# Kernel optimization log

Hardware: AMD Instinct MI355X
Metric: run time of the kernel (lower is better)

Reference implementation:

```python
import jax, jax.numpy as jnp
import numpy as np

N_USER, N_ITEM = 60000, 60000
N = N_USER + N_ITEM
E_BASE = 1500000
P = 200000
IN_DIM, HID, OUT = 128, 128, 64
K_MAX = 0.5


def setup_inputs() -> dict:
    key = jax.random.key(0)
    ks = jax.random.split(key, 20)
    feat_user = jax.random.normal(ks[0], (N_USER, 256), jnp.float32)
    feat_item = jax.random.normal(ks[1], (N_ITEM, 128), jnp.float32)
    src_b = jax.random.randint(ks[2], (E_BASE,), 0, N, jnp.int32)
    dst_b = jax.random.randint(ks[3], (E_BASE,), 0, N, jnp.int32)
    loops = jnp.arange(N, dtype=jnp.int32)  # dgl.add_self_loop
    src = jnp.concatenate([src_b, loops])
    dst = jnp.concatenate([dst_b, loops])
    pos_src = jax.random.randint(ks[4], (P,), 0, N, jnp.int32)
    pos_dst = jax.random.randint(ks[5], (P,), 0, N, jnp.int32)
    neg_src = jax.random.randint(ks[6], (P,), 0, N, jnp.int32)
    neg_dst = jax.random.randint(ks[7], (P,), 0, N, jnp.int32)
    s = 0.05
    W_user = jax.random.normal(ks[8], (256, IN_DIM), jnp.float32) * s
    b_user = jnp.zeros((IN_DIM,), jnp.float32)
    W_item = jax.random.normal(ks[9], (128, IN_DIM), jnp.float32) * s
    b_item = jnp.zeros((IN_DIM,), jnp.float32)
    W_gat = jax.random.normal(ks[10], (IN_DIM, HID), jnp.float32) * s
    attn_l = jax.random.normal(ks[11], (HID,), jnp.float32) * s
    attn_r = jax.random.normal(ks[12], (HID,), jnp.float32) * s
    gat_bias = jnp.zeros((HID,), jnp.float32)
    W_pred = jax.random.normal(ks[13], (HID, OUT), jnp.float32) * s
    b_pred = jnp.zeros((OUT,), jnp.float32)
    return {
        "feat_user": feat_user, "feat_item": feat_item,
        "W_user": W_user, "b_user": b_user, "W_item": W_item, "b_item": b_item,
        "W_gat": W_gat, "attn_l": attn_l, "attn_r": attn_r, "gat_bias": gat_bias,
        "W_pred": W_pred, "b_pred": b_pred,
        "src": src, "dst": dst,
        "pos_src": pos_src, "pos_dst": pos_dst,
        "neg_src": neg_src, "neg_dst": neg_dst,
        "alpha_T": 1,
    }


def _gat_conv(x, src, dst, W_gat, attn_l, attn_r, gat_bias):
    # DGL GATConv, 1 head: fc (no bias), additive attention, edge softmax over dst.
    z = x @ W_gat                              # [N, HID]
    el = z @ attn_l                            # [N]
    er = z @ attn_r                            # [N]
    e = jax.nn.leaky_relu(el[src] + er[dst], 0.2)   # [E]
    m = jax.ops.segment_max(e, dst, num_segments=N)  # per-dst max (self loops -> no empty segs)
    ex = jnp.exp(e - m[dst])
    ssum = jax.ops.segment_sum(ex, dst, num_segments=N)
    a = ex / ssum[dst]                          # edge softmax coeffs
    msg = z[src] * a[:, None]                   # [E, HID]
    out = jax.ops.segment_sum(msg, dst, num_segments=N) + gat_bias
    return jax.nn.elu(out)                      # activation=F.elu


def _hold_loss(score, k_T):
    l = jax.nn.log_sigmoid(score)
    hold = k_T * jnp.max(l)
    l = jnp.where(l > hold, 0.0, l)
    return -jnp.sum(l)


def reference(feat_user, feat_item, W_user, b_user, W_item, b_item,
              W_gat, attn_l, attn_r, gat_bias, W_pred, b_pred,
              src, dst, pos_src, pos_dst, neg_src, neg_dst, alpha_T):
    # per-type input projection then concat in ntype order (dgl.to_homogeneous)
    hu = feat_user @ W_user + b_user
    hi = feat_item @ W_item + b_item
    x = jnp.concatenate([hu, hi], axis=0)       # [N, IN_DIM]
    h = _gat_conv(x, src, dst, W_gat, attn_l, attn_r, gat_bias)
    pos_score = jnp.sum(h[pos_src] * h[pos_dst], axis=1)
    neg_score = jnp.sum(h[neg_src] * h[neg_dst], axis=1)
    k_T = K_MAX if K_MAX <= alpha_T else alpha_T   # k_T = min(k_max, alpha_T)
    loss = _hold_loss(pos_score, k_T) + _hold_loss(neg_score, k_T)
    out = h[:N_USER] @ W_pred + b_pred          # predict_type 'user' == type id 0
    return loss, out
```

## Files before the change

kernel.cpp:

```cpp
#include <hip/hip_runtime.h>
#include <hip/hip_bf16.h>
#include <math.h>

#define NUSER 60000
#define NITEM 60000
#define NNODE 120000
#define BSH 9
#define NB 235
#define CAP 8192

typedef __attribute__((ext_vector_type(8))) short bf16x8;
typedef __attribute__((ext_vector_type(4))) float f32x4;
typedef __attribute__((ext_vector_type(2))) float f32x2;
typedef __attribute__((ext_vector_type(4))) unsigned short u16x4;

__device__ __forceinline__ float leaky02(float x) { return x > 0.f ? x : 0.2f * x; }

__device__ __forceinline__ float inv_ord(unsigned int u) {
  unsigned int bits = (u & 0x80000000u) ? (u & 0x7FFFFFFFu) : ~u;
  return __uint_as_float(bits);
}
__device__ __forceinline__ unsigned int ord_of(float f) {
  unsigned int u = __float_as_uint(f);
  return (u & 0x80000000u) ? ~u : (u | 0x80000000u);
}
__device__ __forceinline__ short f2bs(float f) {
  __hip_bfloat16 h = __float2bfloat16(f);
  return *reinterpret_cast<short*>(&h);
}

__device__ __forceinline__ void f8fma(f32x2& acc, float w, unsigned int u) {
  f32x2 zz = __builtin_amdgcn_cvt_pk_f32_fp8(u, false);
  f32x2 ww; ww.x = w; ww.y = w;
  acc = __builtin_elementwise_fma(ww, zz, acc);
}
__device__ __forceinline__ void fp8dot(f32x2& acc, unsigned int ua, unsigned int ub) {
  f32x2 a0 = __builtin_amdgcn_cvt_pk_f32_fp8(ua, false);
  f32x2 a1 = __builtin_amdgcn_cvt_pk_f32_fp8(ua, true);
  f32x2 b0 = __builtin_amdgcn_cvt_pk_f32_fp8(ub, false);
  f32x2 b1 = __builtin_amdgcn_cvt_pk_f32_fp8(ub, true);
  acc = __builtin_elementwise_fma(a0, b0, acc);
  acc = __builtin_elementwise_fma(a1, b1, acc);
}

__global__ __launch_bounds__(256) void prep_count_kernel(
    const float* __restrict__ Wu, const float* __restrict__ bu, const float* __restrict__ Wi,
    const float* __restrict__ bi, const float* __restrict__ Wg, const float* __restrict__ Wp,
    __hip_bfloat16* __restrict__ Bp_u, __hip_bfloat16* __restrict__ Bp_i,
    __hip_bfloat16* __restrict__ Bp_p, float* __restrict__ bf_u, float* __restrict__ bf_i,
    const int* __restrict__ dst, int* __restrict__ btotal, int E) {
  __shared__ int cnt[NB];
  if (blockIdx.x < 512) {
    int bid = blockIdx.x;
    for (int t = threadIdx.x; t < NB; t += 256) cnt[t] = 0;
    __syncthreads();
    for (int i = bid * 256 + threadIdx.x; i < E; i += 512 * 256)
      atomicAdd(&cnt[dst[i] >> BSH], 1);
    __syncthreads();
    for (int t = threadIdx.x; t < NB; t += 256)
      if (cnt[t]) atomicAdd(&btotal[t], cnt[t]);
    return;
  }
  int t = (blockIdx.x - 512) * 256 + threadIdx.x;
  if (t < 32768) {
    int j = t & 7, lane = (t >> 3) & 63, rest = t >> 9;
    int nt = rest & 7, ks = rest >> 3;
    int k = ks * 32 + ((lane >> 4) << 3) + j;
    int n = nt * 16 + (lane & 15);
    float acc = 0.f;
#pragma unroll 8
    for (int jj = 0; jj < 128; ++jj) acc = fmaf(Wu[k * 128 + jj], Wg[jj * 128 + n], acc);
    Bp_u[t] = __float2bfloat16(acc);
  } else if (t < 49152) {
    int tt = t - 32768;
    int j = tt & 7, lane = (tt >> 3) & 63, rest = tt >> 9;
    int nt = rest & 7, ks = rest >> 3;
    int k = ks * 32 + ((lane >> 4) << 3) + j;
    int n = nt * 16 + (lane & 15);
    float acc = 0.f;
#pragma unroll 8
    for (int jj = 0; jj < 128; ++jj) acc = fmaf(Wi[k * 128 + jj], Wg[jj * 128 + n], acc);
    Bp_i[tt] = __float2bfloat16(acc);
  } else if (t < 57344) {
    int tt = t - 49152;
    int j = tt & 7, lane = (tt >> 3) & 63, rest = tt >> 9;
    int nt = rest & 3, ks = rest >> 2;
    int k = ks * 32 + ((lane >> 4) << 3) + j;
    int n = nt * 16 + (lane & 15);
    Bp_p[tt] = __float2bfloat16(Wp[k * 64 + n]);
  } else if (t < 57344 + 256) {
    int n = t - 57344;
    if (n < 128) {
      float acc = 0.f;
      for (int jj = 0; jj < 128; ++jj) acc = fmaf(bu[jj], Wg[jj * 128 + n], acc);
      bf_u[n] = acc;
    } else {
      int nn = n - 128;
      float acc = 0.f;
      for (int jj = 0; jj < 128; ++jj) acc = fmaf(bi[jj], Wg[jj * 128 + nn], acc);
      bf_i[nn] = acc;
    }
  }
}

__global__ void bscan_kernel(const int* __restrict__ btotal, int* __restrict__ bstart,
                             int* __restrict__ gcur) {
  __shared__ int s[256];
  int t = threadIdx.x;
  int v = (t < NB) ? btotal[t] : 0;
  s[t] = v;
  __syncthreads();
  for (int off = 1; off < 256; off <<= 1) {
    int a = (t >= off) ? s[t - off] : 0;
    __syncthreads();
    s[t] += a;
    __syncthreads();
  }
  int excl = s[t] - v;
  if (t < NB) { bstart[t] = excl; gcur[t] = excl; }
  if (t == NB - 1) bstart[NB] = s[t];
}

template <int K>
__device__ __forceinline__ void zgemm_body(
    char* smem, const float* __restrict__ A, const __hip_bfloat16* __restrict__ Bp,
    const float* __restrict__ bias, const float* __restrict__ al, const float* __restrict__ ar,
    unsigned char* __restrict__ z8, float* __restrict__ el, float* __restrict__ er, int M,
    int blk) {
  const int lane = threadIdx.x & 63, wv = threadIdx.x >> 6;
  const int t = threadIdx.x;
  int arow = blk * 64 + wv * 16 + (lane & 15);
  if (arow >= M) arow = M - 1;
  const float* a0 = A + (size_t)arow * K + ((lane >> 4) << 3);
  const bf16x8* bp = (const bf16x8*)Bp;
  f32x4 acc[8] = {};
#pragma unroll
  for (int ks = 0; ks < K / 32; ++ks) {
    float4 a1 = *(const float4*)(a0 + ks * 32);
    float4 a2 = *(const float4*)(a0 + ks * 32 + 4);
    bf16x8 af;
    af[0] = f2bs(a1.x); af[1] = f2bs(a1.y); af[2] = f2bs(a1.z); af[3] = f2bs(a1.w);
    af[4] = f2bs(a2.x); af[5] = f2bs(a2.y); af[6] = f2bs(a2.z); af[7] = f2bs(a2.w);
#pragma unroll
    for (int nt = 0; nt < 8; ++nt) {
      bf16x8 bfr = bp[(ks * 8 + nt) * 64 + lane];
      acc[nt] = __builtin_amdgcn_mfma_f32_16x16x32_bf16(af, bfr, acc[nt], 0, 0, 0);
    }
  }
  float(*lds2)[68] = (float(*)[68])smem;
  int row = t >> 2, qq = t & 3;
  int gm = blk * 64 + row;
  float pl = 0.f, pr = 0.f;
#pragma unroll
  for (int p = 0; p < 2; ++p) {
    __syncthreads();
#pragma unroll
    for (int nt = p * 4; nt < p * 4 + 4; ++nt) {
      float b = bias[nt * 16 + (lane & 15)];
#pragma unroll
      for (int r = 0; r < 4; ++r)
        lds2[wv * 16 + (lane >> 4) * 4 + r][(nt & 3) * 16 + (lane & 15)] = acc[nt][r] + b;
    }
    __syncthreads();
    if (gm < M) {
#pragma unroll
      for (int v4 = 0; v4 < 2; ++v4) {
        float f[8];
#pragma unroll
        for (int j = 0; j < 8; ++j) {
          f[j] = lds2[row][qq * 16 + v4 * 8 + j];
          int c = p * 64 + qq * 16 + v4 * 8 + j;
          pl = fmaf(f[j], al[c], pl);
          pr = fmaf(f[j], ar[c], pr);
        }
        unsigned int w0 = (unsigned int)__builtin_amdgcn_cvt_pk_fp8_f32(f[0], f[1], 0, false);
        w0 = (unsigned int)__builtin_amdgcn_cvt_pk_fp8_f32(f[2], f[3], (int)w0, true);
        unsigned int w1 = (unsigned int)__builtin_amdgcn_cvt_pk_fp8_f32(f[4], f[5], 0, false);
        w1 = (unsigned int)__builtin_amdgcn_cvt_pk_fp8_f32(f[6], f[7], (int)w1, true);
        uint2 st; st.x = w0; st.y = w1;
        *(uint2*)(z8 + (size_t)gm * 128 + p * 64 + qq * 16 + v4 * 8) = st;
      }
    }
  }
  pl += __shfl_xor(pl, 1, 64); pl += __shfl_xor(pl, 2, 64);
  pr += __shfl_xor(pr, 1, 64); pr += __shfl_xor(pr, 2, 64);
  if (qq == 0 && gm < M) { el[gm] = pl; er[gm] = pr; }
}

__global__ __launch_bounds__(256) void zgemm_scatter_kernel(
    const float* __restrict__ Au, const __hip_bfloat16* __restrict__ Bpu,
    const float* __restrict__ bfu, const float* __restrict__ Ai,
    const __hip_bfloat16* __restrict__ Bpi, const float* __restrict__ bfi,
    const float* __restrict__ al, const float* __restrict__ ar, unsigned char* __restrict__ z8,
    float* __restrict__ el, float* __restrict__ er, int SC, int GU,
    const int* __restrict__ src, const int* __restrict__ dst, int* __restrict__ gcur,
    unsigned int* __restrict__ scratch, int E) {
  __shared__ __align__(16) char smem[17408];
  int bx = blockIdx.x;
  if (bx < SC) {
    int* cnt = (int*)smem;
    int* basep = cnt + NB;
    for (int t = threadIdx.x; t < NB; t += 256) cnt[t] = 0;
    __syncthreads();
    const int i0 = bx * 4096;
    unsigned int v_[16];
    int b_[16], r_[16];
#pragma unroll
    for (int j = 0; j < 16; ++j) {
      int i = i0 + j * 256 + threadIdx.x;
      b_[j] = -1;
      if (i < E) {
        int d = dst[i];
        int s = src[i];
        int b = d >> BSH;
        b_[j] = b;
        r_[j] = atomicAdd(&cnt[b], 1);
        v_[j] = (unsigned int)s | ((unsigned int)(d & 511) << 17);
      }
    }
    __syncthreads();
    for (int t = threadIdx.x; t < NB; t += 256)
      basep[t] = cnt[t] ? atomicAdd(&gcur[t], cnt[t]) : 0;
    __syncthreads();
#pragma unroll
    for (int j = 0; j < 16; ++j)
      if (b_[j] >= 0) scratch[basep[b_[j]] + r_[j]] = v_[j];
    return;
  }
  int gb = bx - SC;
  if (gb < GU)
    zgemm_body<256>(smem, Au, Bpu, bfu, al, ar, z8, el, er, NUSER, gb);
  else
    zgemm_body<128>(smem, Ai, Bpi, bfi, al, ar, z8 + (size_t)NUSER * 128, el + NUSER, er + NUSER,
                    NITEM, gb - GU);
}

__global__ __launch_bounds__(512) void bsort_kernel(const unsigned int* __restrict__ scratch,
                                                    const int* __restrict__ bstart,
                                                    int* __restrict__ offs, int* __restrict__ ssrc) {
  __shared__ unsigned int buf[CAP];
  __shared__ int cnt[512], scn[512], cur[512];
  int b = blockIdx.x, t = threadIdx.x;
  int s = bstart[b], e = bstart[b + 1], n = e - s;
  int d0 = b << BSH;
  int ndst = NNODE - d0;
  if (ndst > 512) ndst = 512;
  cnt[t] = 0;
  cur[t] = 0;
  __syncthreads();
  bool fit = (n <= CAP);
  if (fit) {
    for (int i = t; i < n; i += 512) {
      unsigned int v = scratch[s + i];
      buf[i] = v;
      atomicAdd(&cnt[v >> 17], 1);
    }
  } else {
    for (int i = t; i < n; i += 512) atomicAdd(&cnt[scratch[s + i] >> 17], 1);
  }
  __syncthreads();
  scn[t] = cnt[t];
  __syncthreads();
  for (int off = 1; off < 512; off <<= 1) {
    int a = (t >= off) ? scn[t - off] : 0;
    __syncthreads();
    scn[t] += a;
    __syncthreads();
  }
  int start = scn[t] - cnt[t];
  if (t < ndst) offs[d0 + t] = s + start;
  if (b == NB - 1 && t == 0) offs[NNODE] = e;
  __syncthreads();
  cnt[t] = start;
  __syncthreads();
  if (fit) {
    for (int i = t; i < n; i += 512) {
      unsigned int v = buf[i];
      int dl = v >> 17;
      int r = atomicAdd(&cur[dl], 1);
      ssrc[s + cnt[dl] + r] = (int)(v & 0x1FFFFu);
    }
  } else {
    for (int i = t; i < n; i += 512) {
      unsigned int v = scratch[s + i];
      int dl = v >> 17;
      int r = atomicAdd(&cur[dl], 1);
      ssrc[s + cnt[dl] + r] = (int)(v & 0x1FFFFu);
    }
  }
}

__global__ __launch_bounds__(256) void aggregate_kernel(
    const unsigned char* __restrict__ z8, const float* __restrict__ el,
    const float* __restrict__ er, const int* __restrict__ offs, const int* __restrict__ ssrc,
    const float* __restrict__ gat_bias, __hip_bfloat16* __restrict__ h,
    unsigned char* __restrict__ h8) {
  __shared__ __align__(16) float2 ew[4][128];
  int wv = threadIdx.x >> 6, lane = threadIdx.x & 63;
  int d = blockIdx.x * 4 + wv;
  int s0 = offs[d], s1 = offs[d + 1];
  int deg = s1 - s0;
  float erd = er[d];
  const unsigned short* zw = (const unsigned short*)z8;
  f32x2 acc = {0.f, 0.f};
  float ssum = 0.f;
  if (deg <= 128) {
    float w0 = 0.f, w1 = 0.f;
    int o0 = 0, o1 = 0;
    if (lane < deg) { int s = ssrc[s0 + lane]; o0 = s << 6; w0 = __expf(leaky02(el[s] + erd)); }
    if (64 + lane < deg) { int s = ssrc[s0 + 64 + lane]; o1 = s << 6; w1 = __expf(leaky02(el[s] + erd)); }
    ew[wv][lane] = make_float2(w0, __int_as_float(o0));
    ew[wv][64 + lane] = make_float2(w1, __int_as_float(o1));
    __builtin_amdgcn_wave_barrier();
    int i = 0;
    for (; i + 8 <= deg; i += 8) {
      float4 p0 = *(const float4*)&ew[wv][i];
      float4 p1 = *(const float4*)&ew[wv][i + 2];
      float4 p2 = *(const float4*)&ew[wv][i + 4];
      float4 p3 = *(const float4*)&ew[wv][i + 6];
      unsigned int u0 = zw[__float_as_uint(p0.y) + lane];
      unsigned int u1 = zw[__float_as_uint(p0.w) + lane];
      unsigned int u2 = zw[__float_as_uint(p1.y) + lane];
      unsigned int u3 = zw[__float_as_uint(p1.w) + lane];
      unsigned int u4 = zw[__float_as_uint(p2.y) + lane];
      unsigned int u5 = zw[__float_as_uint(p2.w) + lane];
      unsigned int u6 = zw[__float_as_uint(p3.y) + lane];
      unsigned int u7 = zw[__float_as_uint(p3.w) + lane];
      ssum += ((p0.x + p0.z) + (p1.x + p1.z)) + ((p2.x + p2.z) + (p3.x + p3.z));
      f8fma(acc, p0.x, u0); f8fma(acc, p0.z, u1);
      f8fma(acc, p1.x, u2); f8fma(acc, p1.z, u3);
      f8fma(acc, p2.x, u4); f8fma(acc, p2.z, u5);
      f8fma(acc, p3.x, u6); f8fma(acc, p3.z, u7);
    }
    for (; i + 2 <= deg; i += 2) {
      float4 p = *(const float4*)&ew[wv][i];
      unsigned int ua = zw[__float_as_uint(p.y) + lane];
      unsigned int ub = zw[__float_as_uint(p.w) + lane];
      ssum += p.x + p.z;
      f8fma(acc, p.x, ua); f8fma(acc, p.z, ub);
    }
    if (i < deg) {
      float2 pp = ew[wv][i];
      unsigned int u = zw[__float_as_uint(pp.y) + lane];
      ssum += pp.x;
      f8fma(acc, pp.x, u);
    }
  } else {
    for (int i2 = s0; i2 < s1; ++i2) {
      int s = ssrc[i2];
      float w = __expf(leaky02(el[s] + erd));
      ssum += w;
      unsigned int u = zw[((unsigned int)s << 6) + lane];
      f8fma(acc, w, u);
    }
  }
  float inv = 1.f / ssum;
  float o0f = acc.x * inv + gat_bias[lane * 2];
  float o1f = acc.y * inv + gat_bias[lane * 2 + 1];
  o0f = (o0f > 0.f) ? o0f : (__expf(o0f) - 1.f);
  o1f = (o1f > 0.f) ? o1f : (__expf(o1f) - 1.f);
  ushort2 ov;
  ov.x = (unsigned short)((unsigned int)f2bs(o0f) & 0xFFFFu);
  ov.y = (unsigned short)((unsigned int)f2bs(o1f) & 0xFFFFu);
  *(ushort2*)((unsigned short*)h + (size_t)d * 128 + lane * 2) = ov;
  int pk8 = __builtin_amdgcn_cvt_pk_fp8_f32(o0f, o1f, 0, false);
  *(unsigned short*)(h8 + (size_t)d * 128 + lane * 2) = (unsigned short)(pk8 & 0xFFFF);
}

__global__ __launch_bounds__(256) void scorepred_kernel(
    const unsigned char* __restrict__ h8, const int* __restrict__ ps, const int* __restrict__ pd,
    const int* __restrict__ ns, const int* __restrict__ nd, float* __restrict__ l_pos,
    float* __restrict__ l_neg, unsigned int* __restrict__ maxacc, int P,
    const __hip_bfloat16* __restrict__ h, const __hip_bfloat16* __restrict__ Bp,
    const float* __restrict__ bias, float* __restrict__ outp, int GP, int NSB) {
  if ((int)blockIdx.x < GP) {
    const int lane = threadIdx.x & 63, wv = threadIdx.x >> 6;
    const int m0 = blockIdx.x * 64 + wv * 16;
    int arow = m0 + (lane & 15);
    if (arow >= NUSER) arow = NUSER - 1;
    const bf16x8* a0 = (const bf16x8*)(h + (size_t)arow * 128) + (lane >> 4);
    const bf16x8* bp = (const bf16x8*)Bp;
    f32x4 acc[4] = {};
#pragma unroll
    for (int ks = 0; ks < 4; ++ks) {
      bf16x8 af = a0[ks * 4];
#pragma unroll
      for (int nt = 0; nt < 4; ++nt) {
        bf16x8 bfr = bp[(ks * 4 + nt) * 64 + lane];
        acc[nt] = __builtin_amdgcn_mfma_f32_16x16x32_bf16(af, bfr, acc[nt], 0, 0, 0);
      }
    }
#pragma unroll
    for (int nt = 0; nt < 4; ++nt) {
      int col = nt * 16 + (lane & 15);
      float b = bias[col];
#pragma unroll
      for (int r = 0; r < 4; ++r) {
        int m = m0 + (lane >> 4) * 4 + r;
        if (m < NUSER) outp[(size_t)m * 64 + col] = acc[nt][r] + b;
      }
    }
    return;
  }
  const int sb = blockIdx.x - GP;
  const int g8 = threadIdx.x >> 3, l8 = threadIdx.x & 7;
  const uint4* h4 = (const uint4*)h8;
  const int stride = NSB * 32;
  const int tot = 2 * P;
  float mpos = -1e30f, mneg = -1e30f;

  int i = sb * 32 + g8;
  int aC = 0, bC = 0;
  if (i < tot) {
    bool n = i >= P; int j = n ? i - P : i;
    aC = n ? ns[j] : ps[j]; bC = n ? nd[j] : pd[j];
  }
  uint4 vaC = {0, 0, 0, 0}, vbC = {0, 0, 0, 0};
  if (i < tot) {
    vaC = h4[(size_t)aC * 8 + l8];
    vbC = h4[(size_t)bC * 8 + l8];
  }
  int i1 = i + stride;
  int aN = 0, bN = 0;
  if (i1 < tot) {
    bool n = i1 >= P; int j = n ? i1 - P : i1;
    aN = n ? ns[j] : ps[j]; bN = n ? nd[j] : pd[j];
  }

  while (i < tot) {
    uint4 vaN = {0, 0, 0, 0}, vbN = {0, 0, 0, 0};
    if (i1 < tot) {
      vaN = h4[(size_t)aN * 8 + l8];
      vbN = h4[(size_t)bN * 8 + l8];
    }
    int i2 = i1 + stride;
    int aN2 = 0, bN2 = 0;
    if (i2 < tot) {
      bool n = i2 >= P; int j = n ? i2 - P : i2;
      aN2 = n ? ns[j] : ps[j]; bN2 = n ? nd[j] : pd[j];
    }
    f32x2 acc = {0.f, 0.f};
    fp8dot(acc, vaC.x, vbC.x);
    fp8dot(acc, vaC.y, vbC.y);
    fp8dot(acc, vaC.z, vbC.z);
    fp8dot(acc, vaC.w, vbC.w);
    float s = acc.x + acc.y;
    s += __shfl_xor(s, 1, 8);
    s += __shfl_xor(s, 2, 8);
    s += __shfl_xor(s, 4, 8);
    float lv = fminf(s, 0.f) - log1pf(__expf(-fabsf(s)));
    bool neg = i >= P;
    int j = neg ? i - P : i;
    if (l8 == 0) (neg ? l_neg : l_pos)[j] = lv;
    if (neg) mneg = fmaxf(mneg, lv); else mpos = fmaxf(mpos, lv);
    i = i1; i1 = i2;
    aC = aN; bC = bN; aN = aN2; bN = bN2;
    vaC = vaN; vbC = vbN;
  }
  __shared__ float red0[256], red1[256];
  red0[threadIdx.x] = mpos;
  red1[threadIdx.x] = mneg;
  __syncthreads();
  for (int off = 128; off; off >>= 1) {
    if (threadIdx.x < off) {
      red0[threadIdx.x] = fmaxf(red0[threadIdx.x], red0[threadIdx.x + off]);
      red1[threadIdx.x] = fmaxf(red1[threadIdx.x], red1[threadIdx.x + off]);
    }
    __syncthreads();
  }
  if (threadIdx.x == 0) {
    atomicMax(maxacc + 0, ord_of(red0[0]));
    atomicMax(maxacc + 1, ord_of(red1[0]));
  }
}

__global__ __launch_bounds__(256) void loss_sum_kernel(const float* __restrict__ l_pos,
                                                       const float* __restrict__ l_neg,
                                                       const unsigned int* __restrict__ maxacc,
                                                       const int* __restrict__ alpha,
                                                       float* __restrict__ sums,
                                                       unsigned int* __restrict__ fincnt,
                                                       float* __restrict__ out, int P) {
  __shared__ float sdata[256];
  int which = blockIdx.x >> 9;
  const float* l = which ? l_neg : l_pos;
  float a = (float)alpha[0];
  float kT = (0.5f <= a) ? 0.5f : a;
  float hold = kT * inv_ord(maxacc[which]);
  float s = 0.f;
  for (int i = (blockIdx.x & 511) * 256 + threadIdx.x; i < P; i += 512 * 256) {
    float v = l[i];
    if (!(v > hold)) s += v;
  }
  sdata[threadIdx.x] = s;
  __syncthreads();
  for (int off = 128; off; off >>= 1) {
    if (threadIdx.x < off) sdata[threadIdx.x] += sdata[threadIdx.x + off];
    __syncthreads();
  }
  if (threadIdx.x == 0) {
    atomicAdd(&sums[which], sdata[0]);
    __threadfence();
    unsigned int t = atomicAdd(fincnt, 1u);
    if (t == 1023u) {
      float s0 = atomicAdd(&sums[0], 0.f);
      float s1 = atomicAdd(&sums[1], 0.f);
      out[0] = -(s0 + s1);
    }
  }
}

extern "C" void kernel_launch(void* const* d_in, const int* in_sizes, int n_in,
                              void* d_out, int out_size, void* d_ws, size_t ws_size,
                              hipStream_t stream) {
  const float* feat_user = (const float*)d_in[0];
  const float* feat_item = (const float*)d_in[1];
  const float* W_user = (const float*)d_in[2];
  const float* b_user = (const float*)d_in[3];
  const float* W_item = (const float*)d_in[4];
  const float* b_item = (const float*)d_in[5];
  const float* W_gat = (const float*)d_in[6];
  const float* attn_l = (const float*)d_in[7];
  const float* attn_r = (const float*)d_in[8];
  const float* gat_bias = (const float*)d_in[9];
  const float* W_pred = (const float*)d_in[10];
  const float* b_pred = (const float*)d_in[11];
  const int* src = (const int*)d_in[12];
  const int* dst = (const int*)d_in[13];
  const int* pos_src = (const int*)d_in[14];
  const int* pos_dst = (const int*)d_in[15];
  const int* neg_src = (const int*)d_in[16];
  const int* neg_dst = (const int*)d_in[17];
  const int* alpha = (const int*)d_in[18];
  const int E = in_sizes[12];
  const int P = in_sizes[14];

  char* p = (char*)d_ws;
  auto alloc = [&](size_t bytes) {
    char* r = p;
    p += (bytes + 255) & ~(size_t)255;
    return r;
  };
  unsigned char* z8 = (unsigned char*)alloc((size_t)NNODE * 128);
  __hip_bfloat16* h = (__hip_bfloat16*)alloc((size_t)NNODE * 128 * 2);
  unsigned char* h8 = (unsigned char*)alloc((size_t)NNODE * 128);
  float* el = (float*)alloc((size_t)NNODE * 4);
  float* er = (float*)alloc((size_t)NNODE * 4);
  __hip_bfloat16* Bp_u = (__hip_bfloat16*)alloc(256 * 128 * 2);
  __hip_bfloat16* Bp_i = (__hip_bfloat16*)alloc(128 * 128 * 2);
  __hip_bfloat16* Bp_p = (__hip_bfloat16*)alloc(128 * 64 * 2);
  float* bf_u = (float*)alloc(128 * 4);
  float* bf_i = (float*)alloc(128 * 4);
  int* offs = (int*)alloc((size_t)(NNODE + 4) * 4);
  int* ssrc = (int*)alloc((size_t)E * 4);
  unsigned int* scratch = (unsigned int*)alloc((size_t)E * 4);
  float* l_pos = (float*)alloc((size_t)P * 4);
  float* l_neg = (float*)alloc((size_t)P * 4);
  int* bstart = (int*)alloc((NB + 1) * 4);
  int* gcur = (int*)alloc(NB * 4);
  int* btotal = (int*)alloc((NB + 8) * 4);
  unsigned int* maxacc = (unsigned int*)(btotal + NB);
  float* sums = (float*)(maxacc + 2);
  unsigned int* fincnt = (unsigned int*)(sums + 2);

  hipMemsetAsync(btotal, 0, (NB + 8) * 4, stream);

  prep_count_kernel<<<512 + 225, 256, 0, stream>>>(W_user, b_user, W_item, b_item, W_gat, W_pred,
                                                   Bp_u, Bp_i, Bp_p, bf_u, bf_i, dst, btotal, E);
  bscan_kernel<<<1, 256, 0, stream>>>(btotal, bstart, gcur);
  const int GU = (NUSER + 63) / 64, GI = (NITEM + 63) / 64;
  const int SC = (E + 4095) / 4096;
  zgemm_scatter_kernel<<<SC + GU + GI, 256, 0, stream>>>(feat_user, Bp_u, bf_u, feat_item, Bp_i,
                                                         bf_i, attn_l, attn_r, z8, el, er, SC, GU,
                                                         src, dst, gcur, scratch, E);
  bsort_kernel<<<NB, 512, 0, stream>>>(scratch, bstart, offs, ssrc);
  aggregate_kernel<<<NNODE / 4, 256, 0, stream>>>(z8, el, er, offs, ssrc, gat_bias, h, h8);
  const int GP = (NUSER + 63) / 64;
  const int NSB = 2048;
  scorepred_kernel<<<GP + NSB, 256, 0, stream>>>(h8, pos_src, pos_dst, neg_src, neg_dst, l_pos,
                                                 l_neg, maxacc, P, h, Bp_p, b_pred,
                                                 (float*)d_out + 1, GP, NSB);
  loss_sum_kernel<<<1024, 256, 0, stream>>>(l_pos, l_neg, maxacc, alpha, sums, fincnt,
                                            (float*)d_out, P);

  (void)n_in; (void)out_size; (void)ws_size;
}
```

Baseline: 233.5 us.

## Bucket score pairs by source node to improve gather locality

Counts pos/neg pairs into buckets of 128 source nodes, scans the counts, and scatters the pairs into a bucketed pair buffer alongside the edge scatter. The score kernel then walks one bucket per block, so rows of h8 gathered for the first endpoint fall in a small node range and should hit in cache more often. This adds counting, scan and scatter work plus an extra 8-byte-per-pair buffer. The loss reduction now reads the pos/neg flag from that buffer, which adds another read stream.

```diff
diff --git a/kernel.cpp b/kernel.cpp
--- a/kernel.cpp
+++ b/kernel.cpp
@@ -7,6 +7,8 @@
 #define NNODE 120000
 #define BSH 9
 #define NB 235
+#define PBSH 7
+#define PB 938
 #define CAP 8192
 
 typedef __attribute__((ext_vector_type(8))) short bf16x8;
@@ -48,8 +50,9 @@
     const float* __restrict__ bi, const float* __restrict__ Wg, const float* __restrict__ Wp,
     __hip_bfloat16* __restrict__ Bp_u, __hip_bfloat16* __restrict__ Bp_i,
     __hip_bfloat16* __restrict__ Bp_p, float* __restrict__ bf_u, float* __restrict__ bf_i,
-    const int* __restrict__ dst, int* __restrict__ btotal, int E) {
-  __shared__ int cnt[NB];
+    const int* __restrict__ dst, int* __restrict__ btotal, int E,
+    const int* __restrict__ ps, const int* __restrict__ ns, int* __restrict__ pbtotal, int P) {
+  __shared__ int cnt[PB];
   if (blockIdx.x < 512) {
     int bid = blockIdx.x;
     for (int t = threadIdx.x; t < NB; t += 256) cnt[t] = 0;
@@ -59,6 +62,20 @@
     __syncthreads();
     for (int t = threadIdx.x; t < NB; t += 256)
       if (cnt[t]) atomicAdd(&btotal[t], cnt[t]);
+    return;
+  }
+  if (blockIdx.x >= 737) {
+    int bid = blockIdx.x - 737;
+    int TOT = 2 * P;
+    for (int t = threadIdx.x; t < PB; t += 256) cnt[t] = 0;
+    __syncthreads();
+    for (int i = bid * 256 + threadIdx.x; i < TOT; i += 128 * 256) {
+      int a = (i < P) ? ps[i] : ns[i - P];
+      atomicAdd(&cnt[a >> PBSH], 1);
+    }
+    __syncthreads();
+    for (int t = threadIdx.x; t < PB; t += 256)
+      if (cnt[t]) atomicAdd(&pbtotal[t], cnt[t]);
     return;
   }
   int t = (blockIdx.x - 512) * 256 + threadIdx.x;
@@ -104,7 +121,8 @@
 }
 
 __global__ void bscan_kernel(const int* __restrict__ btotal, int* __restrict__ bstart,
-                             int* __restrict__ gcur) {
+                             int* __restrict__ gcur, const int* __restrict__ pbtotal,
+                             int* __restrict__ pbstart, int* __restrict__ pgcur) {
   __shared__ int s[256];
   int t = threadIdx.x;
   int v = (t < NB) ? btotal[t] : 0;
@@ -119,6 +137,30 @@
   int excl = s[t] - v;
   if (t < NB) { bstart[t] = excl; gcur[t] = excl; }
   if (t == NB - 1) bstart[NB] = s[t];
+  __syncthreads();
+  int v4[4], sum4 = 0;
+#pragma unroll
+  for (int k = 0; k < 4; ++k) {
+    int idx = t * 4 + k;
+    v4[k] = (idx < PB) ? pbtotal[idx] : 0;
+    sum4 += v4[k];
+  }
+  s[t] = sum4;
+  __syncthreads();
+  for (int off = 1; off < 256; off <<= 1) {
+    int a = (t >= off) ? s[t - off] : 0;
+    __syncthreads();
+    s[t] += a;
+    __syncthreads();
+  }
+  int run = s[t] - sum4;
+#pragma unroll
+  for (int k = 0; k < 4; ++k) {
+    int idx = t * 4 + k;
+    if (idx < PB) { pbstart[idx] = run; pgcur[idx] = run; }
+    run += v4[k];
+  }
+  if (t == 255) pbstart[PB] = s[255];
 }
 
 template <int K>
@@ -192,9 +234,11 @@
     const float* __restrict__ bfu, const float* __restrict__ Ai,
     const __hip_bfloat16* __restrict__ Bpi, const float* __restrict__ bfi,
     const float* __restrict__ al, const float* __restrict__ ar, unsigned char* __restrict__ z8,
-    float* __restrict__ el, float* __restrict__ er, int SC, int GU,
+    float* __restrict__ el, float* __restrict__ er, int SC, int PSC, int GU,
     const int* __restrict__ src, const int* __restrict__ dst, int* __restrict__ gcur,
-    unsigned int* __restrict__ scratch, int E) {
+    unsigned int* __restrict__ scratch, int E,
+    const int* __restrict__ ps, const int* __restrict__ pd, const int* __restrict__ ns,
+    const int* __restrict__ nd, int* __restrict__ pgcur, uint2* __restrict__ pairbuf, int P) {
   __shared__ __align__(16) char smem[17408];
   int bx = blockIdx.x;
   if (bx < SC) {
@@ -227,7 +271,40 @@
       if (b_[j] >= 0) scratch[basep[b_[j]] + r_[j]] = v_[j];
     return;
   }
-  int gb = bx - SC;
+  if (bx < SC + PSC) {
+    int* cnt = (int*)smem;
+    int* basep = cnt + PB;
+    for (int t = threadIdx.x; t < PB; t += 256) cnt[t] = 0;
+    __syncthreads();
+    const int TOT = 2 * P;
+    const int i0 = (bx - SC) * 4096;
+    unsigned int x_[16], y_[16];
+    int b_[16], r_[16];
+#pragma unroll
+    for (int j = 0; j < 16; ++j) {
+      int i = i0 + j * 256 + threadIdx.x;
+      b_[j] = -1;
+      if (i < TOT) {
+        int a, b, wh;
+        if (i < P) { a = ps[i]; b = pd[i]; wh = 0; }
+        else { a = ns[i - P]; b = nd[i - P]; wh = 1; }
+        int bk = a >> PBSH;
+        b_[j] = bk;
+        r_[j] = atomicAdd(&cnt[bk], 1);
+        x_[j] = (unsigned int)a | ((unsigned int)wh << 17);
+        y_[j] = (unsigned int)b;
+      }
+    }
+    __syncthreads();
+    for (int t = threadIdx.x; t < PB; t += 256)
+      basep[t] = cnt[t] ? atomicAdd(&pgcur[t], cnt[t]) : 0;
+    __syncthreads();
+#pragma unroll
+    for (int j = 0; j < 16; ++j)
+      if (b_[j] >= 0) pairbuf[basep[b_[j]] + r_[j]] = make_uint2(x_[j], y_[j]);
+    return;
+  }
+  int gb = bx - SC - PSC;
   if (gb < GU)
     zgemm_body<256>(smem, Au, Bpu, bfu, al, ar, z8, el, er, NUSER, gb);
   else
@@ -368,11 +445,11 @@
 }
 
 __global__ __launch_bounds__(256) void scorepred_kernel(
-    const unsigned char* __restrict__ h8, const int* __restrict__ ps, const int* __restrict__ pd,
-    const int* __restrict__ ns, const int* __restrict__ nd, float* __restrict__ l_pos,
-    float* __restrict__ l_neg, unsigned int* __restrict__ maxacc, int P,
+    const unsigned char* __restrict__ h8, const uint2* __restrict__ pairbuf,
+    const int* __restrict__ pbstart, float* __restrict__ l_all,
+    unsigned int* __restrict__ maxacc,
     const __hip_bfloat16* __restrict__ h, const __hip_bfloat16* __restrict__ Bp,
-    const float* __restrict__ bias, float* __restrict__ outp, int GP, int NSB) {
+    const float* __restrict__ bias, float* __restrict__ outp, int GP) {
   if ((int)blockIdx.x < GP) {
     const int lane = threadIdx.x & 63, wv = threadIdx.x >> 6;
     const int m0 = blockIdx.x * 64 + wv * 16;
@@ -405,40 +482,30 @@
   const int sb = blockIdx.x - GP;
   const int g8 = threadIdx.x >> 3, l8 = threadIdx.x & 7;
   const uint4* h4 = (const uint4*)h8;
-  const int stride = NSB * 32;
-  const int tot = 2 * P;
+  const int sP = pbstart[sb], eP = pbstart[sb + 1];
   float mpos = -1e30f, mneg = -1e30f;
 
-  int i = sb * 32 + g8;
-  int aC = 0, bC = 0;
-  if (i < tot) {
-    bool n = i >= P; int j = n ? i - P : i;
-    aC = n ? ns[j] : ps[j]; bC = n ? nd[j] : pd[j];
-  }
+  int i = sP + g8;
+  uint2 prC = make_uint2(0, 0);
   uint4 vaC = {0, 0, 0, 0}, vbC = {0, 0, 0, 0};
-  if (i < tot) {
-    vaC = h4[(size_t)aC * 8 + l8];
-    vbC = h4[(size_t)bC * 8 + l8];
-  }
-  int i1 = i + stride;
-  int aN = 0, bN = 0;
-  if (i1 < tot) {
-    bool n = i1 >= P; int j = n ? i1 - P : i1;
-    aN = n ? ns[j] : ps[j]; bN = n ? nd[j] : pd[j];
-  }
-
-  while (i < tot) {
+  if (i < eP) {
+    prC = pairbuf[i];
+    vaC = h4[(size_t)(prC.x & 0x1FFFFu) * 8 + l8];
+    vbC = h4[(size_t)prC.y * 8 + l8];
+  }
+  int i1 = i + 32;
+  uint2 prN = make_uint2(0, 0);
+  if (i1 < eP) prN = pairbuf[i1];
+
+  while (i < eP) {
     uint4 vaN = {0, 0, 0, 0}, vbN = {0, 0, 0, 0};
-    if (i1 < tot) {
-      vaN = h4[(size_t)aN * 8 + l8];
-      vbN = h4[(size_t)bN * 8 + l8];
-    }
-    int i2 = i1 + stride;
-    int aN2 = 0, bN2 = 0;
-    if (i2 < tot) {
-      bool n = i2 >= P; int j = n ? i2 - P : i2;
-      aN2 = n ? ns[j] : ps[j]; bN2 = n ? nd[j] : pd[j];
-    }
+    if (i1 < eP) {
+      vaN = h4[(size_t)(prN.x & 0x1FFFFu) * 8 + l8];
+      vbN = h4[(size_t)prN.y * 8 + l8];
+    }
+    int i2 = i1 + 32;
+    uint2 prN2 = make_uint2(0, 0);
+    if (i2 < eP) prN2 = pairbuf[i2];
     f32x2 acc = {0.f, 0.f};
     fp8dot(acc, vaC.x, vbC.x);
     fp8dot(acc, vaC.y, vbC.y);
@@ -449,12 +516,11 @@
     s += __shfl_xor(s, 2, 8);
     s += __shfl_xor(s, 4, 8);
     float lv = fminf(s, 0.f) - log1pf(__expf(-fabsf(s)));
-    bool neg = i >= P;
-    int j = neg ? i - P : i;
-    if (l8 == 0) (neg ? l_neg : l_pos)[j] = lv;
+    bool neg = (prC.x >> 17) & 1u;
+    if (l8 == 0) l_all[i] = lv;
     if (neg) mneg = fmaxf(mneg, lv); else mpos = fmaxf(mpos, lv);
     i = i1; i1 = i2;
-    aC = aN; bC = bN; aN = aN2; bN = bN2;
+    prC = prN; prN = prN2;
     vaC = vaN; vbC = vbN;
   }
   __shared__ float red0[256], red1[256];
@@ -469,43 +535,51 @@
     __syncthreads();
   }
   if (threadIdx.x == 0) {
-    atomicMax(maxacc + 0, ord_of(red0[0]));
-    atomicMax(maxacc + 1, ord_of(red1[0]));
-  }
-}
-
-__global__ __launch_bounds__(256) void loss_sum_kernel(const float* __restrict__ l_pos,
-                                                       const float* __restrict__ l_neg,
+    if (red0[0] > -1e29f) atomicMax(maxacc + 0, ord_of(red0[0]));
+    if (red1[0] > -1e29f) atomicMax(maxacc + 1, ord_of(red1[0]));
+  }
+}
+
+__global__ __launch_bounds__(256) void loss_sum_kernel(const float* __restrict__ l_all,
+                                                       const uint2* __restrict__ pairbuf,
                                                        const unsigned int* __restrict__ maxacc,
                                                        const int* __restrict__ alpha,
                                                        float* __restrict__ sums,
                                                        unsigned int* __restrict__ fincnt,
-                                                       float* __restrict__ out, int P) {
-  __shared__ float sdata[256];
-  int which = blockIdx.x >> 9;
-  const float* l = which ? l_neg : l_pos;
+                                                       float* __restrict__ out, int TOT) {
+  __shared__ float sd0[256], sd1[256];
   float a = (float)alpha[0];
   float kT = (0.5f <= a) ? 0.5f : a;
-  float hold = kT * inv_ord(maxacc[which]);
-  float s = 0.f;
-  for (int i = (blockIdx.x & 511) * 256 + threadIdx.x; i < P; i += 512 * 256) {
-    float v = l[i];
-    if (!(v > hold)) s += v;
-  }
-  sdata[threadIdx.x] = s;
+  float hold0 = kT * inv_ord(maxacc[0]);
+  float hold1 = kT * inv_ord(maxacc[1]);
+  float s0 = 0.f, s1 = 0.f;
+  for (int i = blockIdx.x * 256 + threadIdx.x; i < TOT; i += gridDim.x * 256) {
+    float v = l_all[i];
+    if ((pairbuf[i].x >> 17) & 1u) {
+      if (!(v > hold1)) s1 += v;
+    } else {
+      if (!(v > hold0)) s0 += v;
+    }
+  }
+  sd0[threadIdx.x] = s0;
+  sd1[threadIdx.x] = s1;
   __syncthreads();
   for (int off = 128; off; off >>= 1) {
-    if (threadIdx.x < off) sdata[threadIdx.x] += sdata[threadIdx.x + off];
+    if (threadIdx.x < off) {
+      sd0[threadIdx.x] += sd0[threadIdx.x + off];
+      sd1[threadIdx.x] += sd1[threadIdx.x + off];
+    }
     __syncthreads();
   }
   if (threadIdx.x == 0) {
-    atomicAdd(&sums[which], sdata[0]);
+    atomicAdd(&sums[0], sd0[0]);
+    atomicAdd(&sums[1], sd1[0]);
     __threadfence();
     unsigned int t = atomicAdd(fincnt, 1u);
-    if (t == 1023u) {
-      float s0 = atomicAdd(&sums[0], 0.f);
-      float s1 = atomicAdd(&sums[1], 0.f);
-      out[0] = -(s0 + s1);
+    if (t == gridDim.x - 1) {
+      float f0 = atomicAdd(&sums[0], 0.f);
+      float f1 = atomicAdd(&sums[1], 0.f);
+      out[0] = -(f0 + f1);
     }
   }
 }
@@ -534,6 +608,7 @@
   const int* alpha = (const int*)d_in[18];
   const int E = in_sizes[12];
   const int P = in_sizes[14];
+  const int TOT = 2 * P;
 
   char* p = (char*)d_ws;
   auto alloc = [&](size_t bytes) {
@@ -554,34 +629,37 @@
   int* offs = (int*)alloc((size_t)(NNODE + 4) * 4);
   int* ssrc = (int*)alloc((size_t)E * 4);
   unsigned int* scratch = (unsigned int*)alloc((size_t)E * 4);
-  float* l_pos = (float*)alloc((size_t)P * 4);
-  float* l_neg = (float*)alloc((size_t)P * 4);
+  uint2* pairbuf = (uint2*)alloc((size_t)TOT * 8);
+  float* l_all = (float*)alloc((size_t)TOT * 4);
   int* bstart = (int*)alloc((NB + 1) * 4);
   int* gcur = (int*)alloc(NB * 4);
-  int* btotal = (int*)alloc((NB + 8) * 4);
-  unsigned int* maxacc = (unsigned int*)(btotal + NB);
+  int* pbstart = (int*)alloc((PB + 1) * 4);
+  int* pgcur = (int*)alloc(PB * 4);
+  int* btotal = (int*)alloc((NB + PB + 8) * 4);
+  int* pbtotal = btotal + NB;
+  unsigned int* maxacc = (unsigned int*)(pbtotal + PB);
   float* sums = (float*)(maxacc + 2);
   unsigned int* fincnt = (unsigned int*)(sums + 2);
 
-  hipMemsetAsync(btotal, 0, (NB + 8) * 4, stream);
-
-  prep_count_kernel<<<512 + 225, 256, 0, stream>>>(W_user, b_user, W_item, b_item, W_gat, W_pred,
-                                                   Bp_u, Bp_i, Bp_p, bf_u, bf_i, dst, btotal, E);
-  bscan_kernel<<<1, 256, 0, stream>>>(btotal, bstart, gcur);
+  hipMemsetAsync(btotal, 0, (NB + PB + 8) * 4, stream);
+
+  prep_count_kernel<<<512 + 225 + 128, 256, 0, stream>>>(
+      W_user, b_user, W_item, b_item, W_gat, W_pred, Bp_u, Bp_i, Bp_p, bf_u, bf_i, dst, btotal, E,
+      pos_src, neg_src, pbtotal, P);
+  bscan_kernel<<<1, 256, 0, stream>>>(btotal, bstart, gcur, pbtotal, pbstart, pgcur);
   const int GU = (NUSER + 63) / 64, GI = (NITEM + 63) / 64;
   const int SC = (E + 4095) / 4096;
-  zgemm_scatter_kernel<<<SC + GU + GI, 256, 0, stream>>>(feat_user, Bp_u, bf_u, feat_item, Bp_i,
-                                                         bf_i, attn_l, attn_r, z8, el, er, SC, GU,
-                                                         src, dst, gcur, scratch, E);
+  const int PSC = (TOT + 4095) / 4096;
+  zgemm_scatter_kernel<<<SC + PSC + GU + GI, 256, 0, stream>>>(
+      feat_user, Bp_u, bf_u, feat_item, Bp_i, bf_i, attn_l, attn_r, z8, el, er, SC, PSC, GU, src,
+      dst, gcur, scratch, E, pos_src, pos_dst, neg_src, neg_dst, pgcur, pairbuf, P);
   bsort_kernel<<<NB, 512, 0, stream>>>(scratch, bstart, offs, ssrc);
   aggregate_kernel<<<NNODE / 4, 256, 0, stream>>>(z8, el, er, offs, ssrc, gat_bias, h, h8);
   const int GP = (NUSER + 63) / 64;
-  const int NSB = 2048;
-  scorepred_kernel<<<GP + NSB, 256, 0, stream>>>(h8, pos_src, pos_dst, neg_src, neg_dst, l_pos,
-                                                 l_neg, maxacc, P, h, Bp_p, b_pred,
-                                                 (float*)d_out + 1, GP, NSB);
-  loss_sum_kernel<<<1024, 256, 0, stream>>>(l_pos, l_neg, maxacc, alpha, sums, fincnt,
-                                            (float*)d_out, P);
+  scorepred_kernel<<<GP + PB, 256, 0, stream>>>(h8, pairbuf, pbstart, l_all, maxacc, h, Bp_p,
+                                                b_pred, (float*)d_out + 1, GP);
+  loss_sum_kernel<<<1024, 256, 0, stream>>>(l_all, pairbuf, maxacc, alpha, sums, fincnt,
+                                            (float*)d_out, TOT);
 
   (void)n_in; (void)out_size; (void)ws_size;
 }
```

After: 233.3 us. About the same (-0.1%).
